# Kernel tuning notes

Hardware: AMD Instinct MI355X
Metric: run time of the kernel (lower is better)

The kernel has to match this reference:

```python
import jax, jax.numpy as jnp
import numpy as np

VOC_SIZE = 32768
DIM = 512
NUM_TOPK = 64
BATCH = 4096


def setup_inputs() -> dict:
    key = jax.random.key(0)
    ks = jax.random.split(key, 8)
    lim = 1.0 / np.sqrt(DIM)  # kaiming_uniform(a=sqrt(5)) on [V, d] -> U(-1/sqrt(d), 1/sqrt(d))
    x = jax.random.normal(ks[0], (BATCH, DIM), dtype=jnp.float32)
    codebook = jax.random.uniform(ks[1], (VOC_SIZE, DIM), dtype=jnp.float32, minval=-lim, maxval=lim)
    Wq = jax.random.uniform(ks[2], (DIM, DIM), dtype=jnp.float32, minval=-lim, maxval=lim)
    bq = jax.random.uniform(ks[3], (DIM,), dtype=jnp.float32, minval=-lim, maxval=lim)
    Wk = jax.random.uniform(ks[4], (DIM, DIM), dtype=jnp.float32, minval=-lim, maxval=lim)
    bk = jax.random.uniform(ks[5], (DIM,), dtype=jnp.float32, minval=-lim, maxval=lim)
    Wv = jax.random.uniform(ks[6], (DIM, DIM), dtype=jnp.float32, minval=-lim, maxval=lim)
    bv = jax.random.uniform(ks[7], (DIM,), dtype=jnp.float32, minval=-lim, maxval=lim)
    return {"x": x, "codebook": codebook, "Wq": Wq, "bq": bq,
            "Wk": Wk, "bk": bk, "Wv": Wv, "bv": bv}


def reference(x, codebook, Wq, bq, Wk, bk, Wv, bv):
    # projections (torch Linear with weight stored pre-transposed as [in, out])
    q = x @ Wq + bq              # [B, d]
    k = codebook @ Wk + bk       # [V, d]
    v = codebook @ Wv + bv       # [V, d]

    dots = jnp.einsum('bd,kd->bk', q, k)              # [B, V]
    top, _ = jax.lax.top_k(dots, NUM_TOPK)            # [B, num_topk]
    thresh = top[..., -1:]                            # k-th largest value per row
    mask_value = -jnp.finfo(dots.dtype).max
    dots = jnp.where(dots < thresh, mask_value, dots)
    attn = jax.nn.softmax(dots, axis=-1)              # [B, V]
    out = jnp.einsum('bk,kd->bd', attn, v)            # [B, d]
    return out
```

## Files before the change

### kernel.cpp

```cpp
#include <hip/hip_runtime.h>
#include <cstdint>

#define VOC   32768
#define DIM   512
#define TOPK  64
#define BATCH 4096

#define KSIG     2.45f
#define EPS_SEL  0.012f
#define CAND_CAP 512
#define RES_CAP  256
#define FCAP     1024

typedef unsigned short u16;
typedef __attribute__((ext_vector_type(8))) short bf16x8;
typedef __attribute__((ext_vector_type(4))) float f32x4;

__device__ __forceinline__ u16 f2bf(float f) {
    unsigned u = __float_as_uint(f);
    unsigned r = (u + 0x7FFFu + ((u >> 16) & 1u)) >> 16;
    return (u16)r;
}
__device__ __forceinline__ float bf2f(u16 h) {
    return __uint_as_float(((unsigned)h) << 16);
}
__device__ __forceinline__ unsigned enc16(u16 h) {
    return (h & 0x8000u) ? (unsigned)((u16)~h) : (unsigned)(h | 0x8000u);
}
__device__ __forceinline__ float dec16(unsigned s16) {
    u16 h = (s16 & 0x8000u) ? (u16)(s16 ^ 0x8000u) : (u16)(~s16);
    return bf2f(h);
}

__device__ __forceinline__ void async16(const void* g, void* l) {
    __builtin_amdgcn_global_load_lds(
        (const __attribute__((address_space(1))) void*)g,
        (__attribute__((address_space(3))) void*)l, 16, 0, 0);
}

template <bool BT, bool F64ACC>
__global__ __launch_bounds__(256)
void gemm64(const float* __restrict__ A, const float* __restrict__ B,
            const float* __restrict__ bias, float* __restrict__ C,
            int M, int N, int K)
{
    const int KS = 16;
    __shared__ float As[KS][68];
    __shared__ float Bs[KS][64];

    const int tid = threadIdx.x;
    const int m0 = blockIdx.y * 64;
    const int n0 = blockIdx.x * 64;
    const int ty = tid >> 4;
    const int tx = tid & 15;

    float acc[4][4];
    double acc64[4][4];
#pragma unroll
    for (int i = 0; i < 4; i++)
#pragma unroll
        for (int j = 0; j < 4; j++) { acc[i][j] = 0.f; if (F64ACC) acc64[i][j] = 0.0; }

    for (int kt = 0; kt < K; kt += KS) {
        {
            int row = tid >> 2, kq = tid & 3;
            const float4 av = *(const float4*)(A + (size_t)(m0 + row) * K + kt + kq * 4);
            As[kq * 4 + 0][row] = av.x;
            As[kq * 4 + 1][row] = av.y;
            As[kq * 4 + 2][row] = av.z;
            As[kq * 4 + 3][row] = av.w;
        }
        if (!BT) {
            int krow = tid >> 4, nq = tid & 15;
            *(float4*)&Bs[krow][nq * 4] =
                *(const float4*)(B + (size_t)(kt + krow) * N + n0 + nq * 4);
        } else {
            int nrow = tid >> 2, kq = tid & 3;
            const float4 bv = *(const float4*)(B + (size_t)(n0 + nrow) * K + kt + kq * 4);
            Bs[kq * 4 + 0][nrow] = bv.x;
            Bs[kq * 4 + 1][nrow] = bv.y;
            Bs[kq * 4 + 2][nrow] = bv.z;
            Bs[kq * 4 + 3][nrow] = bv.w;
        }
        __syncthreads();

#pragma unroll
        for (int kk = 0; kk < KS; kk++) {
            float4 a = *(const float4*)&As[kk][ty * 4];
            float4 b = *(const float4*)&Bs[kk][tx * 4];
            float av[4] = {a.x, a.y, a.z, a.w};
            float bv[4] = {b.x, b.y, b.z, b.w};
#pragma unroll
            for (int i = 0; i < 4; i++)
#pragma unroll
                for (int j = 0; j < 4; j++)
                    acc[i][j] += av[i] * bv[j];
        }
        __syncthreads();
        if (F64ACC) {
#pragma unroll
            for (int i = 0; i < 4; i++)
#pragma unroll
                for (int j = 0; j < 4; j++) { acc64[i][j] += (double)acc[i][j]; acc[i][j] = 0.f; }
        }
    }

    float4 bb = make_float4(0.f, 0.f, 0.f, 0.f);
    if (bias) bb = *(const float4*)(bias + n0 + tx * 4);
#pragma unroll
    for (int i = 0; i < 4; i++) {
        float4 o;
        o.x = (F64ACC ? (float)acc64[i][0] : acc[i][0]) + bb.x;
        o.y = (F64ACC ? (float)acc64[i][1] : acc[i][1]) + bb.y;
        o.z = (F64ACC ? (float)acc64[i][2] : acc[i][2]) + bb.z;
        o.w = (F64ACC ? (float)acc64[i][3] : acc[i][3]) + bb.w;
        *(float4*)(C + (size_t)(m0 + ty * 4 + i) * N + n0 + tx * 4) = o;
    }
}

__global__ void bias_fold(const float* __restrict__ bq, const float* __restrict__ Wk,
                          float* __restrict__ bqk)
{
    int j = blockIdx.x * 256 + threadIdx.x;
    if (j >= DIM) return;
    double s = 0.0;
    const float* wr = Wk + (size_t)j * DIM;
    for (int d = 0; d < DIM; d++) s += (double)bq[d] * (double)wr[d];
    bqk[j] = (float)s;
}

__global__ void zero_ws(unsigned* __restrict__ p, int n)
{
    int i = blockIdx.x * 256 + threadIdx.x;
    if (i < n) p[i] = 0u;
}

__global__ __launch_bounds__(256)
void cbar_accum(const float* __restrict__ cb, float* __restrict__ cbarsum)
{
    const int tid = threadIdx.x;
    const int r0 = blockIdx.x * 128;
    float s0 = 0.f, s1 = 0.f;
    for (int r = 0; r < 128; r++) {
        const float* rp = cb + (size_t)(r0 + r) * DIM;
        s0 += rp[tid];
        s1 += rp[tid + 256];
    }
    atomicAdd(&cbarsum[tid], s0);
    atomicAdd(&cbarsum[tid + 256], s1);
}

__global__ __launch_bounds__(256)
void rowstats(const float* __restrict__ q2, const float* __restrict__ cbarsum,
              float* __restrict__ trow, float* __restrict__ sigrow)
{
    const int tid = threadIdx.x, lane = tid & 63, wave = tid >> 6;
    const int row = blockIdx.x * 4 + wave;
    const float* qp = q2 + (size_t)row * DIM + lane * 8;
    float4 a0 = *(const float4*)qp, a1 = *(const float4*)(qp + 4);
    const float* cp = cbarsum + lane * 8;
    float4 c0 = *(const float4*)cp, c1 = *(const float4*)(cp + 4);
    float mu = a0.x*c0.x + a0.y*c0.y + a0.z*c0.z + a0.w*c0.w
             + a1.x*c1.x + a1.y*c1.y + a1.z*c1.z + a1.w*c1.w;
    float nr = a0.x*a0.x + a0.y*a0.y + a0.z*a0.z + a0.w*a0.w
             + a1.x*a1.x + a1.y*a1.y + a1.z*a1.z + a1.w*a1.w;
#pragma unroll
    for (int off = 32; off > 0; off >>= 1) {
        mu += __shfl_down(mu, off);
        nr += __shfl_down(nr, off);
    }
    if (lane == 0) {
        mu *= (1.f / VOC);
        float sig = sqrtf(nr * (1.f / 1536.f));
        trow[row] = mu + KSIG * sig;
        sigrow[row] = sig;
    }
}

__global__ __launch_bounds__(256)
void pack_rows(const float* __restrict__ src, u16* __restrict__ hi,
               u16* __restrict__ lo, int R, int log2R)
{
    int idx = blockIdx.x * 256 + threadIdx.x;
    int c8  = idx >> log2R;
    int row = idx & (R - 1);
    const float* sp = src + (size_t)row * DIM + c8 * 8;
    float xv[8];
    *(float4*)&xv[0] = *(const float4*)sp;
    *(float4*)&xv[4] = *(const float4*)(sp + 4);
    int ks = c8 >> 2, ch = c8 & 3;
    size_t ob = ((size_t)(ks * 4 + ch) * R + row) * 8;
    u16 h[8], l[8];
#pragma unroll
    for (int j = 0; j < 8; j++) {
        h[j] = f2bf(xv[j]);
        l[j] = f2bf(xv[j] - bf2f(h[j]));
    }
    *(uint4*)(hi + ob) = *(const uint4*)h;
    if (lo) *(uint4*)(lo + ob) = *(const uint4*)l;
}

__global__ __launch_bounds__(256)
void pack_bT(const float* __restrict__ W, u16* __restrict__ hi, u16* __restrict__ lo)
{
    int idx = blockIdx.x * 256 + threadIdx.x;
    int n  = idx & (DIM - 1);
    int c8 = idx >> 9;
    int ks = c8 >> 2, ch = c8 & 3;
    size_t ob = ((size_t)(ks * 4 + ch) * DIM + n) * 8;
    u16 h[8], l[8];
#pragma unroll
    for (int j = 0; j < 8; j++) {
        float x = W[(size_t)(c8 * 8 + j) * DIM + n];
        h[j] = f2bf(x);
        l[j] = f2bf(x - bf2f(h[j]));
    }
    *(uint4*)(hi + ob) = *(const uint4*)h;
    *(uint4*)(lo + ob) = *(const uint4*)l;
}

__global__ __launch_bounds__(256, 4)
void mfma_dots(const u16* __restrict__ Ah, const u16* __restrict__ Bh,
               const float* __restrict__ trow, unsigned* __restrict__ candBuf,
               unsigned* __restrict__ counters)
{
    __shared__ u16 lds[2 * 8192];

    const int tid  = threadIdx.x;
    const int lane = tid & 63;
    const int wave = tid >> 6;
    const int wm = wave >> 1, wn = wave & 1;
    const int lr = lane & 15;
    const int q  = lane >> 4;

    const int L   = blockIdx.x;
    const int xcd = L & 7;
    const int j   = L >> 3;
    const int m0  = (xcd * 4 + (j & 3)) * 128;
    const int n0  = (j >> 2) * 128;

    const int a  = wave >> 1;
    const u16* src = a ? Bh : Ah;
    const int rb   = a ? n0 : m0;
    const size_t R = a ? (size_t)VOC : (size_t)BATCH;
    const int i0   = (wave & 1) * 4;

#define ISSUE(ks, b)                                                          \
    {                                                                         \
        _Pragma("unroll")                                                     \
        for (int s_ = 0; s_ < 4; s_++) {                                      \
            int i_ = i0 + s_;                                                 \
            const u16* gp_ = src + ((size_t)((ks) * 4 + (i_ >> 1)) * R + rb   \
                                    + (i_ & 1) * 64 + lane) * 8;              \
            async16(gp_, &lds[(b) * 8192 + a * 4096 + i_ * 512 + lane * 8]);  \
        }                                                                     \
    }

    f32x4 acc[4][4] = {};

    ISSUE(0, 0)

    for (int s = 0; s < 16; s++) {
        __builtin_amdgcn_s_waitcnt(0x0F70);
        __builtin_amdgcn_s_barrier();
        if (s < 15) ISSUE(s + 1, (s + 1) & 1)
        const u16* base = &lds[(s & 1) * 8192];

        bf16x8 ah[4];
#pragma unroll
        for (int mt = 0; mt < 4; mt++)
            ah[mt] = *(const bf16x8*)&base[q * 1024 + (wm * 64 + mt * 16 + lr) * 8];
#pragma unroll
        for (int nt = 0; nt < 4; nt++) {
            bf16x8 bh = *(const bf16x8*)&base[4096 + q * 1024 + (wn * 64 + nt * 16 + lr) * 8];
#pragma unroll
            for (int mt = 0; mt < 4; mt++)
                acc[mt][nt] = __builtin_amdgcn_mfma_f32_16x16x32_bf16(ah[mt], bh, acc[mt][nt], 0, 0, 0);
        }
    }
#undef ISSUE

#pragma unroll
    for (int mt = 0; mt < 4; mt++) {
#pragma unroll
        for (int r = 0; r < 4; r++) {
            int rowg = m0 + wm * 64 + mt * 16 + q * 4 + r;
            float tr = trow[rowg];
#pragma unroll
            for (int nt = 0; nt < 4; nt++) {
                float val = acc[mt][nt][r];
                if (val >= tr) {
                    unsigned slot = atomicAdd(&counters[rowg], 1u);
                    if (slot < CAND_CAP) {
                        unsigned s16 = enc16(f2bf(val));
                        candBuf[(size_t)rowg * CAND_CAP + slot] =
                            (s16 << 16) | (unsigned)(n0 + wn * 64 + nt * 16 + lr);
                    }
                }
            }
        }
    }
}

__global__ __launch_bounds__(256, 2)
void mfma_out(const u16* __restrict__ Ah, const u16* __restrict__ Al,
              const u16* __restrict__ Bh, const u16* __restrict__ Bl,
              const float* __restrict__ bias, float* __restrict__ Cout, int Ma)
{
    __shared__ u16 lds[2 * 16384];

    const int tid  = threadIdx.x;
    const int lane = tid & 63;
    const int wave = tid >> 6;
    const int wm = wave >> 1, wn = wave & 1;
    const int m0 = blockIdx.y * 128, n0 = blockIdx.x * 128;
    const int lr = lane & 15;
    const int q  = lane >> 4;

    f32x4 acc[4][4] = {};
    const u16* garr[4] = {Ah, Bh, Al, Bl};
    const int a = wave;
    const u16* src = garr[a];
    const bool isA = (a == 0 || a == 2);
    const int rb = isA ? m0 : n0;
    const size_t R = isA ? (size_t)Ma : (size_t)DIM;

#define VISSUE(ks, b)                                                         \
    {                                                                         \
        _Pragma("unroll")                                                     \
        for (int i_ = 0; i_ < 8; i_++) {                                      \
            const u16* gp_ = src + ((size_t)((ks) * 4 + (i_ >> 1)) * R + rb   \
                                    + (i_ & 1) * 64 + lane) * 8;              \
            async16(gp_, &lds[(b) * 16384 + a * 4096 + i_ * 512 + lane * 8]); \
        }                                                                     \
    }

    VISSUE(0, 0)

    for (int ks = 0; ks < 16; ks++) {
        __syncthreads();
        if (ks < 15) VISSUE(ks + 1, (ks + 1) & 1)
        const u16* base = &lds[(ks & 1) * 16384];

        bf16x8 ah[4], al[4];
#pragma unroll
        for (int mt = 0; mt < 4; mt++) {
            int row = wm * 64 + mt * 16 + lr;
            ah[mt] = *(const bf16x8*)&base[0 * 4096 + q * 1024 + row * 8];
            al[mt] = *(const bf16x8*)&base[2 * 4096 + q * 1024 + row * 8];
        }
#pragma unroll
        for (int nt = 0; nt < 4; nt++) {
            int col = wn * 64 + nt * 16 + lr;
            bf16x8 bh = *(const bf16x8*)&base[1 * 4096 + q * 1024 + col * 8];
            bf16x8 bl = *(const bf16x8*)&base[3 * 4096 + q * 1024 + col * 8];
#pragma unroll
            for (int mt = 0; mt < 4; mt++) {
                acc[mt][nt] = __builtin_amdgcn_mfma_f32_16x16x32_bf16(ah[mt], bh, acc[mt][nt], 0, 0, 0);
                acc[mt][nt] = __builtin_amdgcn_mfma_f32_16x16x32_bf16(ah[mt], bl, acc[mt][nt], 0, 0, 0);
                acc[mt][nt] = __builtin_amdgcn_mfma_f32_16x16x32_bf16(al[mt], bh, acc[mt][nt], 0, 0, 0);
            }
        }
    }
#undef VISSUE

#pragma unroll
    for (int mt = 0; mt < 4; mt++)
#pragma unroll
        for (int nt = 0; nt < 4; nt++) {
            int col = n0 + wn * 64 + nt * 16 + lr;
            float bb = bias[col];
#pragma unroll
            for (int r = 0; r < 4; r++) {
                int rowg = m0 + wm * 64 + mt * 16 + q * 4 + r;
                Cout[(size_t)rowg * DIM + col] = acc[mt][nt][r] + bb;
            }
        }
}

__global__ __launch_bounds__(256)
void select6(const unsigned* __restrict__ candBuf, const unsigned* __restrict__ counters,
             const float* __restrict__ trow, const float* __restrict__ q2,
             const float* __restrict__ codebook, float* __restrict__ y,
             unsigned* __restrict__ flags)
{
    __shared__ unsigned recs[CAND_CAP];
    __shared__ unsigned long long keys[RES_CAP];
    __shared__ float q2s[DIM];
    __shared__ float wArr[RES_CAP];
    __shared__ float redf[256];
    __shared__ unsigned redu[256];
    __shared__ unsigned s_R;

    const int tid  = threadIdx.x;
    const int lane = tid & 63;
    const int wave = tid >> 6;
    const int row  = blockIdx.x;

    const unsigned cnt = counters[row];
    if (cnt < TOPK || cnt > CAND_CAP) {
        if (tid == 0) flags[row] = 1u;
        return;
    }
    for (int i = tid; i < DIM; i += 256) q2s[i] = q2[(size_t)row * DIM + i];
    for (int i = tid; i < CAND_CAP; i += 256)
        recs[i] = (i < (int)cnt) ? candBuf[(size_t)row * CAND_CAP + i] : 0u;
    if (tid == 0) s_R = 0;
    __syncthreads();

    for (int k = 2; k <= CAND_CAP; k <<= 1) {
        for (int j = k >> 1; j > 0; j >>= 1) {
#pragma unroll
            for (int e = 0; e < 2; e++) {
                int i = tid + e * 256;
                int ixj = i ^ j;
                if (ixj > i) {
                    unsigned a = recs[i], b = recs[ixj];
                    if (((i & k) == 0) ? (a < b) : (a > b)) { recs[i] = b; recs[ixj] = a; }
                }
            }
            __syncthreads();
        }
    }

    const float a64  = dec16(recs[TOPK - 1] >> 16);
    const float band = a64 - 2.f * EPS_SEL;
    if (trow[row] > band) {
        if (tid == 0) flags[row] = 1u;
        return;
    }

#pragma unroll
    for (int e = 0; e < 2; e++) {
        int i = tid + e * 256;
        if (i < (int)cnt && dec16(recs[i] >> 16) >= band) atomicAdd(&s_R, 1u);
    }
    __syncthreads();
    const int R = (int)s_R;
    if (R > RES_CAP) {
        if (tid == 0) flags[row] = 1u;
        return;
    }

    for (int c = wave; c < R; c += 4) {
        unsigned idx = recs[c] & 0xFFFFu;
        const float* cb = codebook + (size_t)idx * DIM + lane * 8;
        float4 c0 = *(const float4*)cb, c1 = *(const float4*)(cb + 4);
        const float* qp = &q2s[lane * 8];
        float4 a0 = *(const float4*)qp, a1 = *(const float4*)(qp + 4);
        double s = (double)a0.x * c0.x + (double)a0.y * c0.y
                 + (double)a0.z * c0.z + (double)a0.w * c0.w
                 + (double)a1.x * c1.x + (double)a1.y * c1.y
                 + (double)a1.z * c1.z + (double)a1.w * c1.w;
#pragma unroll
        for (int off = 32; off > 0; off >>= 1) s += __shfl_down(s, off);
        if (lane == 0) {
            float val = (float)s;
            unsigned b = __float_as_uint(val);
            unsigned sk = (b & 0x80000000u) ? ~b : (b | 0x80000000u);
            keys[c] = ((unsigned long long)(~sk) << 32) | idx;
        }
    }
    if (tid >= R && tid < RES_CAP) keys[tid] = ~0ULL;
    __syncthreads();

    for (int k = 2; k <= RES_CAP; k <<= 1) {
        for (int j = k >> 1; j > 0; j >>= 1) {
            int ixj = tid ^ j;
            if (ixj > tid) {
                unsigned long long a = keys[tid], b2 = keys[ixj];
                if (((tid & k) == 0) ? (a > b2) : (a < b2)) { keys[tid] = b2; keys[ixj] = a; }
            }
            __syncthreads();
        }
    }

    const unsigned threshInv = (unsigned)(keys[TOPK - 1] >> 32);
    unsigned sk0 = ~(unsigned)(keys[0] >> 32);
    const float vmax = __uint_as_float((sk0 & 0x80000000u) ? (sk0 & 0x7FFFFFFFu) : ~sk0);

    unsigned hi = (unsigned)(keys[tid] >> 32);
    bool sel = (hi <= threshInv);
    unsigned sk = ~hi;
    float val = __uint_as_float((sk & 0x80000000u) ? (sk & 0x7FFFFFFFu) : ~sk);
    float w = sel ? expf(val - vmax) : 0.f;
    wArr[tid] = w;
    redf[tid] = w;
    redu[tid] = sel ? 1u : 0u;
    __syncthreads();
    for (int s = 128; s > 0; s >>= 1) {
        if (tid < s) { redf[tid] += redf[tid + s]; redu[tid] += redu[tid + s]; }
        __syncthreads();
    }
    const float invZ = 1.0f / redf[0];
    const int selCount = (int)redu[0];

    for (int d = tid; d < DIM; d += 256) {
        float acc = 0.f;
        for (int i = 0; i < selCount; i++) {
            unsigned idx = (unsigned)(keys[i] & 0xFFFFFFFFu);
            acc += wArr[i] * codebook[(size_t)idx * DIM + d];
        }
        y[(size_t)row * DIM + d] = acc * invZ;
    }
}

__global__ __launch_bounds__(256)
void fallback_row(const unsigned* __restrict__ flags, const float* __restrict__ q2,
                  const float* __restrict__ codebook, const float* __restrict__ trow,
                  const float* __restrict__ sigrow, float* __restrict__ y)
{
    const int row = blockIdx.x;
    if (!flags[row]) return;

    __shared__ float q2s[DIM];
    __shared__ unsigned long long keys[FCAP];
    __shared__ float wArr[FCAP];
    __shared__ float redf[256];
    __shared__ unsigned redu[256];
    __shared__ unsigned s_cnt;

    const int tid = threadIdx.x;
    for (int i = tid; i < DIM; i += 256) q2s[i] = q2[(size_t)row * DIM + i];
    const float sig = sigrow[row];
    float tf = trow[row] - 0.35f * sig;
    unsigned cnt = 0;

    for (int it = 0; it < 16; it++) {
        if (tid == 0) s_cnt = 0;
        __syncthreads();
        for (int i = tid; i < VOC; i += 256) {
            const float* cb = codebook + (size_t)i * DIM;
            double s = 0.0;
            for (int d = 0; d < DIM; d += 4) {
                float4 c4 = *(const float4*)(cb + d);
                s += (double)q2s[d + 0] * (double)c4.x + (double)q2s[d + 1] * (double)c4.y
                   + (double)q2s[d + 2] * (double)c4.z + (double)q2s[d + 3] * (double)c4.w;
            }
            float vv = (float)s;
            if (vv >= tf) {
                unsigned p = atomicAdd(&s_cnt, 1u);
                if (p < FCAP) {
                    unsigned b = __float_as_uint(vv);
                    unsigned sk = (b & 0x80000000u) ? ~b : (b | 0x80000000u);
                    keys[p] = ((unsigned long long)(~sk) << 32) | (unsigned)i;
                }
            }
        }
        __syncthreads();
        cnt = s_cnt;
        if (cnt > FCAP) { tf += 0.15f * sig; continue; }
        if (cnt < TOPK) { tf -= 0.35f * sig; continue; }
        break;
    }
    if (cnt > FCAP) cnt = FCAP;
    for (int i = tid; i < FCAP; i += 256)
        if (i >= (int)cnt) keys[i] = ~0ULL;
    __syncthreads();

    for (int k = 2; k <= FCAP; k <<= 1) {
        for (int j = k >> 1; j > 0; j >>= 1) {
#pragma unroll
            for (int e = 0; e < 4; e++) {
                int i = tid + e * 256;
                int ixj = i ^ j;
                if (ixj > i) {
                    unsigned long long a = keys[i], b = keys[ixj];
                    if (((i & k) == 0) ? (a > b) : (a < b)) { keys[i] = b; keys[ixj] = a; }
                }
            }
            __syncthreads();
        }
    }

    const unsigned threshInv = (unsigned)(keys[TOPK - 1] >> 32);
    unsigned sk0 = ~(unsigned)(keys[0] >> 32);
    const float vmax = __uint_as_float((sk0 & 0x80000000u) ? (sk0 & 0x7FFFFFFFu) : ~sk0);

    float lsum = 0.f; unsigned lcnt = 0;
    for (int i = tid; i < FCAP; i += 256) {
        unsigned hi = (unsigned)(keys[i] >> 32);
        bool sel = (hi <= threshInv);
        unsigned sk = ~hi;
        float vv = __uint_as_float((sk & 0x80000000u) ? (sk & 0x7FFFFFFFu) : ~sk);
        float w = sel ? expf(vv - vmax) : 0.f;
        wArr[i] = w;
        lsum += w; lcnt += sel ? 1u : 0u;
    }
    redf[tid] = lsum; redu[tid] = lcnt;
    __syncthreads();
    for (int s = 128; s > 0; s >>= 1) {
        if (tid < s) { redf[tid] += redf[tid + s]; redu[tid] += redu[tid + s]; }
        __syncthreads();
    }
    const float invZ = 1.f / redf[0];
    const int selCount = (int)redu[0];

    for (int d = tid; d < DIM; d += 256) {
        float acc = 0.f;
        for (int i = 0; i < selCount; i++) {
            unsigned idx = (unsigned)(keys[i] & 0xFFFFFFFFu);
            acc += wArr[i] * codebook[(size_t)idx * DIM + d];
        }
        y[(size_t)row * DIM + d] = acc * invZ;
    }
}

extern "C" void kernel_launch(void* const* d_in, const int* in_sizes, int n_in,
                              void* d_out, int out_size, void* d_ws, size_t ws_size,
                              hipStream_t stream)
{
    const float* x        = (const float*)d_in[0];
    const float* codebook = (const float*)d_in[1];
    const float* Wq       = (const float*)d_in[2];
    const float* bq       = (const float*)d_in[3];
    const float* Wk       = (const float*)d_in[4];
    const float* Wv       = (const float*)d_in[6];
    const float* bv       = (const float*)d_in[7];
    float* out = (float*)d_out;

    float* q2   = (float*)d_ws;
    float* Wqk  = q2   + (size_t)BATCH * DIM;
    float* bqk  = Wqk  + (size_t)DIM * DIM;
    float* y    = bqk  + 1024;
    float* trow = y    + (size_t)BATCH * DIM;
    float* sigr = trow + BATCH;
    unsigned* counters = (unsigned*)(sigr + BATCH);
    unsigned* flags    = counters + BATCH;
    float* cbarsum     = (float*)(flags + BATCH);
    unsigned* candBuf  = (unsigned*)(cbarsum + 512);
    u16* q2h = (u16*)(candBuf + (size_t)BATCH * CAND_CAP);
    u16* cbh = q2h + (size_t)BATCH * DIM;
    u16* yh  = cbh + (size_t)VOC * DIM;
    u16* yl  = yh  + (size_t)BATCH * DIM;
    u16* wvh = yl  + (size_t)BATCH * DIM;
    u16* wvl = wvh + (size_t)DIM * DIM;

    dim3 blk(256);

    zero_ws<<<dim3(34), blk, 0, stream>>>(counters, BATCH * 2 + 512);

    gemm64<true, true><<<dim3(DIM / 64, DIM / 64), blk, 0, stream>>>(
        Wq, Wk, nullptr, Wqk, DIM, DIM, DIM);
    bias_fold<<<dim3(2), blk, 0, stream>>>(bq, Wk, bqk);
    gemm64<false, true><<<dim3(DIM / 64, BATCH / 64), blk, 0, stream>>>(
        x, Wqk, bqk, q2, BATCH, DIM, DIM);

    cbar_accum<<<dim3(VOC / 128), blk, 0, stream>>>(codebook, cbarsum);
    rowstats<<<dim3(BATCH / 4), blk, 0, stream>>>(q2, cbarsum, trow, sigr);

    pack_rows<<<dim3(BATCH * 64 / 256), blk, 0, stream>>>(q2, q2h, nullptr, BATCH, 12);
    pack_rows<<<dim3(VOC * 64 / 256), blk, 0, stream>>>(codebook, cbh, nullptr, VOC, 15);
    pack_bT<<<dim3(DIM * 64 / 256), blk, 0, stream>>>(Wv, wvh, wvl);

    mfma_dots<<<dim3(8192), blk, 0, stream>>>(q2h, cbh, trow, candBuf, counters);

    select6<<<dim3(BATCH), blk, 0, stream>>>(
        candBuf, counters, trow, q2, codebook, y, flags);
    fallback_row<<<dim3(BATCH), blk, 0, stream>>>(
        flags, q2, codebook, trow, sigr, y);

    pack_rows<<<dim3(BATCH * 64 / 256), blk, 0, stream>>>(y, yh, yl, BATCH, 12);
    mfma_out<<<dim3(DIM / 128, BATCH / 128), blk, 0, stream>>>(
        yh, yl, wvh, wvl, bv, out, BATCH);
}
```

Before: 705.4 us.

## Radix-select threshold, MFMA q-projection, pointer-increment loads and setprio

The full 512-element bitonic sort of each row's candidates in select6 is replaced by a two-pass 8-bit radix histogram that finds the 64th-largest key. Survivors within the band are compacted into a separate list. The fp32 q-projection GEMM is replaced by a split-bf16 MFMA GEMM that packs x and Wqk first, reusing existing buffers as scratch. The main dots kernel now advances precomputed global pointers instead of recomputing addresses, and raises wave priority around its MFMA block. The split-bf16 projection may change precision slightly, and the scratch aliasing relies on buffer lifetimes not overlapping.

After: 678.9 us. -3.8%, faster.

```diff
diff --git a/kernel.cpp b/kernel.cpp
--- a/kernel.cpp
+++ b/kernel.cpp
@@ -245,31 +245,39 @@
     const size_t R = a ? (size_t)VOC : (size_t)BATCH;
     const int i0   = (wave & 1) * 4;
 
-#define ISSUE(ks, b)                                                          \
+    const size_t gstep = (size_t)4 * R * 8;
+    const u16* gp0 = src + ((size_t)(((i0 + 0) >> 1)) * R + rb + ((i0 + 0) & 1) * 64 + lane) * 8;
+    const u16* gp1 = src + ((size_t)(((i0 + 1) >> 1)) * R + rb + ((i0 + 1) & 1) * 64 + lane) * 8;
+    const u16* gp2 = src + ((size_t)(((i0 + 2) >> 1)) * R + rb + ((i0 + 2) & 1) * 64 + lane) * 8;
+    const u16* gp3 = src + ((size_t)(((i0 + 3) >> 1)) * R + rb + ((i0 + 3) & 1) * 64 + lane) * 8;
+    const int loff0 = a * 4096 + (i0 + 0) * 512 + lane * 8;
+    const int loff1 = a * 4096 + (i0 + 1) * 512 + lane * 8;
+    const int loff2 = a * 4096 + (i0 + 2) * 512 + lane * 8;
+    const int loff3 = a * 4096 + (i0 + 3) * 512 + lane * 8;
+
+#define ISSUE(b)                                                              \
     {                                                                         \
-        _Pragma("unroll")                                                     \
-        for (int s_ = 0; s_ < 4; s_++) {                                      \
-            int i_ = i0 + s_;                                                 \
-            const u16* gp_ = src + ((size_t)((ks) * 4 + (i_ >> 1)) * R + rb   \
-                                    + (i_ & 1) * 64 + lane) * 8;              \
-            async16(gp_, &lds[(b) * 8192 + a * 4096 + i_ * 512 + lane * 8]);  \
-        }                                                                     \
+        async16(gp0, &lds[(b) * 8192 + loff0]); gp0 += gstep;                 \
+        async16(gp1, &lds[(b) * 8192 + loff1]); gp1 += gstep;                 \
+        async16(gp2, &lds[(b) * 8192 + loff2]); gp2 += gstep;                 \
+        async16(gp3, &lds[(b) * 8192 + loff3]); gp3 += gstep;                 \
     }
 
     f32x4 acc[4][4] = {};
 
-    ISSUE(0, 0)
+    ISSUE(0)
 
     for (int s = 0; s < 16; s++) {
         __builtin_amdgcn_s_waitcnt(0x0F70);
         __builtin_amdgcn_s_barrier();
-        if (s < 15) ISSUE(s + 1, (s + 1) & 1)
+        if (s < 15) ISSUE((s + 1) & 1)
         const u16* base = &lds[(s & 1) * 8192];
 
         bf16x8 ah[4];
 #pragma unroll
         for (int mt = 0; mt < 4; mt++)
             ah[mt] = *(const bf16x8*)&base[q * 1024 + (wm * 64 + mt * 16 + lr) * 8];
+        __builtin_amdgcn_s_setprio(1);
 #pragma unroll
         for (int nt = 0; nt < 4; nt++) {
             bf16x8 bh = *(const bf16x8*)&base[4096 + q * 1024 + (wn * 64 + nt * 16 + lr) * 8];
@@ -277,6 +285,7 @@
             for (int mt = 0; mt < 4; mt++)
                 acc[mt][nt] = __builtin_amdgcn_mfma_f32_16x16x32_bf16(ah[mt], bh, acc[mt][nt], 0, 0, 0);
         }
+        __builtin_amdgcn_s_setprio(0);
     }
 #undef ISSUE
 
@@ -385,12 +394,15 @@
              unsigned* __restrict__ flags)
 {
     __shared__ unsigned recs[CAND_CAP];
+    __shared__ unsigned list[RES_CAP];
+    __shared__ unsigned hist[256];
     __shared__ unsigned long long keys[RES_CAP];
     __shared__ float q2s[DIM];
     __shared__ float wArr[RES_CAP];
     __shared__ float redf[256];
     __shared__ unsigned redu[256];
     __shared__ unsigned s_R;
+    __shared__ unsigned s_b1, s_rem, s_thr;
 
     const int tid  = threadIdx.x;
     const int lane = tid & 63;
@@ -406,24 +418,48 @@
     for (int i = tid; i < CAND_CAP; i += 256)
         recs[i] = (i < (int)cnt) ? candBuf[(size_t)row * CAND_CAP + i] : 0u;
     if (tid == 0) s_R = 0;
-    __syncthreads();
-
-    for (int k = 2; k <= CAND_CAP; k <<= 1) {
-        for (int j = k >> 1; j > 0; j >>= 1) {
-#pragma unroll
-            for (int e = 0; e < 2; e++) {
-                int i = tid + e * 256;
-                int ixj = i ^ j;
-                if (ixj > i) {
-                    unsigned a = recs[i], b = recs[ixj];
-                    if (((i & k) == 0) ? (a < b) : (a > b)) { recs[i] = b; recs[ixj] = a; }
-                }
-            }
-            __syncthreads();
-        }
-    }
-
-    const float a64  = dec16(recs[TOPK - 1] >> 16);
+    hist[tid] = 0;
+    __syncthreads();
+
+#pragma unroll
+    for (int e = 0; e < 2; e++) {
+        int i = tid + e * 256;
+        if (i < (int)cnt) atomicAdd(&hist[recs[i] >> 24], 1u);
+    }
+    __syncthreads();
+    if (tid == 0) {
+        unsigned c = 0; int b = 255;
+        for (; b > 0; b--) {
+            unsigned h = hist[b];
+            if (c + h >= TOPK) break;
+            c += h;
+        }
+        s_b1 = (unsigned)b; s_rem = TOPK - c;
+    }
+    __syncthreads();
+    const unsigned b1 = s_b1, rem = s_rem;
+    hist[tid] = 0;
+    __syncthreads();
+
+#pragma unroll
+    for (int e = 0; e < 2; e++) {
+        int i = tid + e * 256;
+        if (i < (int)cnt && (recs[i] >> 24) == b1)
+            atomicAdd(&hist[(recs[i] >> 16) & 0xFFu], 1u);
+    }
+    __syncthreads();
+    if (tid == 0) {
+        unsigned c = 0; int b = 255;
+        for (; b > 0; b--) {
+            unsigned h = hist[b];
+            if (c + h >= rem) break;
+            c += h;
+        }
+        s_thr = (b1 << 8) | (unsigned)b;
+    }
+    __syncthreads();
+
+    const float a64  = dec16(s_thr);
     const float band = a64 - 2.f * EPS_SEL;
     if (trow[row] > band) {
         if (tid == 0) flags[row] = 1u;
@@ -433,7 +469,10 @@
 #pragma unroll
     for (int e = 0; e < 2; e++) {
         int i = tid + e * 256;
-        if (i < (int)cnt && dec16(recs[i] >> 16) >= band) atomicAdd(&s_R, 1u);
+        if (i < (int)cnt && dec16(recs[i] >> 16) >= band) {
+            unsigned p = atomicAdd(&s_R, 1u);
+            if (p < RES_CAP) list[p] = recs[i];
+        }
     }
     __syncthreads();
     const int R = (int)s_R;
@@ -443,7 +482,7 @@
     }
 
     for (int c = wave; c < R; c += 4) {
-        unsigned idx = recs[c] & 0xFFFFu;
+        unsigned idx = list[c] & 0xFFFFu;
         const float* cb = codebook + (size_t)idx * DIM + lane * 8;
         float4 c0 = *(const float4*)cb, c1 = *(const float4*)(cb + 4);
         const float* qp = &q2s[lane * 8];
@@ -636,15 +675,23 @@
     u16* wvh = yl  + (size_t)BATCH * DIM;
     u16* wvl = wvh + (size_t)DIM * DIM;
 
+    u16* xh   = yh;
+    u16* xl   = yl;
+    u16* wqkh = (u16*)candBuf;
+    u16* wqkl = wqkh + (size_t)DIM * DIM;
+
     dim3 blk(256);
-
-    zero_ws<<<dim3(34), blk, 0, stream>>>(counters, BATCH * 2 + 512);
 
     gemm64<true, true><<<dim3(DIM / 64, DIM / 64), blk, 0, stream>>>(
         Wq, Wk, nullptr, Wqk, DIM, DIM, DIM);
     bias_fold<<<dim3(2), blk, 0, stream>>>(bq, Wk, bqk);
-    gemm64<false, true><<<dim3(DIM / 64, BATCH / 64), blk, 0, stream>>>(
-        x, Wqk, bqk, q2, BATCH, DIM, DIM);
+
+    pack_bT<<<dim3(DIM * 64 / 256), blk, 0, stream>>>(Wqk, wqkh, wqkl);
+    pack_rows<<<dim3(BATCH * 64 / 256), blk, 0, stream>>>(x, xh, xl, BATCH, 12);
+    mfma_out<<<dim3(DIM / 128, BATCH / 128), blk, 0, stream>>>(
+        xh, xl, wqkh, wqkl, bqk, q2, BATCH);
+
+    zero_ws<<<dim3(34), blk, 0, stream>>>(counters, BATCH * 2 + 512);
 
     cbar_accum<<<dim3(VOC / 128), blk, 0, stream>>>(codebook, cbarsum);
     rowstats<<<dim3(BATCH / 4), blk, 0, stream>>>(q2, cbarsum, trow, sigr);
```
